# Optimization experiments

Measured on AMD Instinct MI355X. Metric: run time of the kernel, lower is better.

## Reference

```python
import jax, jax.numpy as jnp
import numpy as np

N_NODES = 10000
N_EDGES = 160000
MAX_K = 8
IN_NF = 64
HID = 64
ED = 16
HEADS = 4
NVEC = 5

def _mlp2_silu(x, w1, b1, w2, b2):
    # Linear -> SiLU -> Linear -> SiLU
    return jax.nn.silu(jax.nn.silu(x @ w1 + b1) @ w2 + b2)

def _mlp_out(x, w1, b1, w2, b2):
    # Linear -> SiLU -> Linear
    return jax.nn.silu(x @ w1 + b1) @ w2 + b2

def _segment_mean(data, ids, n):
    s = jax.ops.segment_sum(data, ids, num_segments=n)
    c = jax.ops.segment_sum(jnp.ones_like(data), ids, num_segments=n)
    return s / jnp.maximum(c, 1.0)

def setup_inputs() -> dict:
    key = jax.random.key(0)
    ks = jax.random.split(key, 48)
    p = lambda k, shape: jax.random.normal(k, shape, dtype=jnp.float32) * 0.05
    inp = {
        "h": jax.random.normal(ks[0], (N_NODES, IN_NF), dtype=jnp.float32),
        "coord": jax.random.normal(ks[1], (N_NODES, 3), dtype=jnp.float32),
        "edges": jax.random.randint(ks[2], (2, N_EDGES), 0, N_NODES),
        "nvecs": jax.random.normal(ks[3], (N_NODES, NVEC, 3), dtype=jnp.float32),
        "edge_attr": jax.random.normal(ks[4], (N_EDGES, ED), dtype=jnp.float32),
        "node_attr": jax.random.normal(ks[5], (N_NODES, HID), dtype=jnp.float32),
        "init_coord": jax.random.normal(ks[6], (N_NODES, 3), dtype=jnp.float32),
    }
    kidx = jax.random.randint(ks[7], (N_EDGES, 2, MAX_K), 0, N_EDGES)
    red = jax.random.uniform(ks[8], (N_EDGES, MAX_K)) < 0.2
    inp["klist"] = jnp.where(red[:, None, :], -1, kidx)
    chem_in = 2 * IN_NF + 2 * HID + ED
    pos_in = NVEC + 15 + ED  # edge_coords_nf(20) + edges_in_d
    inp.update({
        "w_chem1": p(ks[9], (chem_in, HID)), "b_chem1": jnp.zeros((HID,), jnp.float32),
        "w_chem2": p(ks[10], (HID, HID)), "b_chem2": jnp.zeros((HID,), jnp.float32),
        "w_pos1": p(ks[11], (pos_in, HID)), "b_pos1": jnp.zeros((HID,), jnp.float32),
        "w_pos2": p(ks[12], (HID, HID)), "b_pos2": jnp.zeros((HID,), jnp.float32),
        "w_sh": p(ks[13], (HID, HID)), "b_sh": jnp.zeros((HID,), jnp.float32),
        "w_att": p(ks[14], (HID, 1)), "b_att": jnp.zeros((1,), jnp.float32),
        "wq": p(ks[15], (HEADS, HID, HID)),
        "wk": p(ks[16], (HEADS, HID, HID)),
        "wv": p(ks[17], (HEADS, HID, HID)),
        "wb": p(ks[18], (HEADS, HID)),
        "wg": p(ks[19], (HEADS, HID, HID)), "bg": jnp.zeros((HEADS, HID), jnp.float32),
        "w_out": p(ks[20], (HEADS * HID, HID)), "b_out": jnp.zeros((HID,), jnp.float32),
        "wu1": p(ks[21], (HID, HID)), "bu1": jnp.zeros((HID,), jnp.float32),
        "wu2": p(ks[22], (HID, 1)), "bu2": jnp.zeros((1,), jnp.float32),
        "wx1": p(ks[23], (HID, HID)), "bx1": jnp.zeros((HID,), jnp.float32),
        "wx2": p(ks[24], (HID, 1)), "bx2": jnp.zeros((1,), jnp.float32),
        "wh1": p(ks[25], (2 * HID + IN_NF, HID)), "bh1": jnp.zeros((HID,), jnp.float32),
        "wh2": p(ks[26], (HID, HID)), "bh2": jnp.zeros((HID,), jnp.float32),
    })
    return inp

def reference(h, coord, edges, nvecs, edge_attr, node_attr, init_coord, klist,
              w_chem1, b_chem1, w_chem2, b_chem2, w_pos1, b_pos1, w_pos2, b_pos2,
              w_sh, b_sh, w_att, b_att, wq, wk, wv, wb, wg, bg, w_out, b_out,
              wu1, bu1, wu2, bu2, wx1, bx1, wx2, bx2, wh1, bh1, wh2, bh2):
    row, col = edges[0], edges[1]
    # radial features + normalized coordinate differences
    cd = coord[row] - coord[col]
    cd = cd / (jnp.linalg.norm(cd, axis=-1, keepdims=True) + 1e-8)
    init_radial = jnp.sum(cd ** 2, axis=1, keepdims=True)                 # (E, 1)
    radial = jnp.exp(init_radial * (-0.5 / 2.25 ** jnp.arange(15.0)))     # (E, 15)
    nprod = jnp.sum(nvecs[row] * nvecs[col], axis=-1)                     # (E, NVEC)
    chem = _mlp2_silu(jnp.concatenate([h[row], h[col], node_attr[row], node_attr[col], edge_attr], axis=1),
                      w_chem1, b_chem1, w_chem2, b_chem2)
    pos = _mlp2_silu(jnp.concatenate([nprod, radial, edge_attr], axis=1),
                     w_pos1, b_pos1, w_pos2, b_pos2)
    z = jax.nn.silu(chem @ w_sh + b_sh) * pos
    z = z * jax.nn.sigmoid(z @ w_att + b_att)
    # triangle k-NN attention over edges
    idx_i2k, idx_j2k = klist[:, 0], klist[:, 1]                           # (E, K)
    red = idx_i2k == -1
    heads = []
    for hd in range(HEADS):
        q = z @ wq[hd]; k_ = z @ wk[hd]; v = z @ wv[hd]; b = z @ wb[hd]
        g = jax.nn.sigmoid(z @ wg[hd] + bg[hd])
        tri_k = jnp.where(red[:, :, None], 0.0, k_[idx_i2k])              # (E, K, HID)
        tri_b = jnp.where(red, 0.0, b[idx_j2k])                           # (E, K)
        tri_v = v[idx_i2k]                                                # (E, K, HID)
        alpha = jnp.einsum('ed,ekd->ek', q, tri_k) / np.sqrt(HID) + tri_b
        alpha = jax.nn.softmax(jnp.where(red, -10000.0, alpha), axis=1)
        heads.append(g * jnp.einsum('ek,ekd->ed', alpha, tri_v))
    m = jnp.concatenate(heads, axis=-1) @ w_out + b_out
    # equivariant coordinate update
    ita = 0.2
    x_trans = cd * (_mlp_out(chem, wu1, bu1, wu2, bu2) * _mlp_out(pos, wx1, bx1, wx2, bx2))
    x_agg = _segment_mean(x_trans, row, N_NODES)
    coord_new = ita * init_coord + (1.0 - ita) * coord + x_agg
    m_agg = _segment_mean(m, row, N_NODES)
    h_new = h + _mlp_out(jnp.concatenate([h, node_attr, m_agg], axis=-1), wh1, bh1, wh2, bh2)
    return (h_new, coord_new)
```

## Files before the change

kernel.cpp:

```cpp
#include <hip/hip_runtime.h>
#include <math.h>

#define NE 160000
#define NN 10000

#define DEV __device__ __forceinline__

typedef float v2f __attribute__((ext_vector_type(2)));
typedef __attribute__((ext_vector_type(8))) short bf16x8;
typedef __attribute__((ext_vector_type(4))) float f32x4;

DEV float fsilu(float x) { return x / (1.0f + __expf(-x)); }
DEV float fsig(float x)  { return 1.0f / (1.0f + __expf(-x)); }

DEV unsigned pack2(float a, float b) {
  unsigned ua = __float_as_uint(a); ua += 0x7FFFu + ((ua >> 16) & 1u);
  unsigned ub = __float_as_uint(b); ub += 0x7FFFu + ((ub >> 16) & 1u);
  return (ua >> 16) | (ub & 0xFFFF0000u);
}

DEV unsigned packf8_4(float a, float b, float c, float d) {
  int r = __builtin_amdgcn_cvt_pk_fp8_f32(a, b, 0, false);
  r = __builtin_amdgcn_cvt_pk_fp8_f32(c, d, r, true);
  return (unsigned)r;
}
template<bool HI>
DEV v2f up2(unsigned u) { return __builtin_amdgcn_cvt_pk_f32_fp8((int)u, HI); }

DEV float dot16p(uint4 u, const float* q) {
  v2f f; float a = 0.f, b = 0.f;
  f = up2<false>(u.x); a = fmaf(f.x, q[0],  a); b = fmaf(f.y, q[1],  b);
  f = up2<true >(u.x); a = fmaf(f.x, q[2],  a); b = fmaf(f.y, q[3],  b);
  f = up2<false>(u.y); a = fmaf(f.x, q[4],  a); b = fmaf(f.y, q[5],  b);
  f = up2<true >(u.y); a = fmaf(f.x, q[6],  a); b = fmaf(f.y, q[7],  b);
  f = up2<false>(u.z); a = fmaf(f.x, q[8],  a); b = fmaf(f.y, q[9],  b);
  f = up2<true >(u.z); a = fmaf(f.x, q[10], a); b = fmaf(f.y, q[11], b);
  f = up2<false>(u.w); a = fmaf(f.x, q[12], a); b = fmaf(f.y, q[13], b);
  f = up2<true >(u.w); a = fmaf(f.x, q[14], a); b = fmaf(f.y, q[15], b);
  return a + b;
}
DEV void acc16(uint4 u, float pk, float* o) {
  v2f f;
  f = up2<false>(u.x); o[0]  = fmaf(pk, f.x, o[0]);  o[1]  = fmaf(pk, f.y, o[1]);
  f = up2<true >(u.x); o[2]  = fmaf(pk, f.x, o[2]);  o[3]  = fmaf(pk, f.y, o[3]);
  f = up2<false>(u.y); o[4]  = fmaf(pk, f.x, o[4]);  o[5]  = fmaf(pk, f.y, o[5]);
  f = up2<true >(u.y); o[6]  = fmaf(pk, f.x, o[6]);  o[7]  = fmaf(pk, f.y, o[7]);
  f = up2<false>(u.z); o[8]  = fmaf(pk, f.x, o[8]);  o[9]  = fmaf(pk, f.y, o[9]);
  f = up2<true >(u.z); o[10] = fmaf(pk, f.x, o[10]); o[11] = fmaf(pk, f.y, o[11]);
  f = up2<false>(u.w); o[12] = fmaf(pk, f.x, o[12]); o[13] = fmaf(pk, f.y, o[13]);
  f = up2<true >(u.w); o[14] = fmaf(pk, f.x, o[14]); o[15] = fmaf(pk, f.y, o[15]);
}

DEV void ldrow16(const unsigned* __restrict__ p, unsigned (&r)[16]) {
#pragma unroll
  for (int t = 0; t < 4; ++t) {
    uint4 u = ((const uint4*)p)[t];
    r[4*t] = u.x; r[4*t+1] = u.y; r[4*t+2] = u.z; r[4*t+3] = u.w;
  }
}
DEV void unpackf8_32(const unsigned (&p)[8], float (&o)[32]) {
#pragma unroll
  for (int t = 0; t < 8; ++t) {
    v2f f0 = up2<false>(p[t]);
    v2f f1 = up2<true >(p[t]);
    o[4*t+0] = f0.x; o[4*t+1] = f0.y; o[4*t+2] = f1.x; o[4*t+3] = f1.y;
  }
}
DEV void store32(float* dst, const float (&a)[32]) {
#pragma unroll
  for (int j = 0; j < 32; j += 4)
    *(float4*)(dst + j) = make_float4(a[j], a[j+1], a[j+2], a[j+3]);
}

DEV bf16x8 packrow8(const float* __restrict__ p) {
  float4 a = *(const float4*)p;
  float4 b = *(const float4*)(p + 4);
  uint4 u = make_uint4(pack2(a.x, a.y), pack2(a.z, a.w),
                       pack2(b.x, b.y), pack2(b.z, b.w));
  return __builtin_bit_cast(bf16x8, u);
}

DEV void mm4(const unsigned short* __restrict__ wm, int er, int q,
             const bf16x8 (&bfr)[2], f32x4 (&acc)[4]) {
#pragma unroll
  for (int nf = 0; nf < 4; ++nf) {
    const unsigned short* ar = wm + (size_t)(nf * 16 + er) * 64 + q * 8;
    const bf16x8 a0 = *(const bf16x8*)ar;
    const bf16x8 a1 = *(const bf16x8*)(ar + 32);
    acc[nf] = __builtin_amdgcn_mfma_f32_16x16x32_bf16(a0, bfr[0], acc[nf], 0, 0, 0);
    acc[nf] = __builtin_amdgcn_mfma_f32_16x16x32_bf16(a1, bfr[1], acc[nf], 0, 0, 0);
  }
}

__global__ void __launch_bounds__(256)
k_count(const int* __restrict__ edges, int* __restrict__ icnt) {
  int e = blockIdx.x * 256 + threadIdx.x;
  if (e < NE) atomicAdd(&icnt[edges[e]], 1);
}

__global__ void __launch_bounds__(256)
k_scan(const int* __restrict__ icnt, int* __restrict__ ioffs) {
  __shared__ int part[256];
  const int t = threadIdx.x;
  const int base = t * 40;
  int loc[40];
  int s = 0;
#pragma unroll
  for (int i = 0; i < 40; ++i) {
    int idx = base + i;
    int v = (idx < NN) ? icnt[idx] : 0;
    loc[i] = v; s += v;
  }
  part[t] = s;
  __syncthreads();
  for (int off = 1; off < 256; off <<= 1) {
    int v = (t >= off) ? part[t - off] : 0;
    __syncthreads();
    part[t] += v;
    __syncthreads();
  }
  int run = (t == 0) ? 0 : part[t - 1];
#pragma unroll
  for (int i = 0; i < 40; ++i) {
    int idx = base + i;
    if (idx < NN) { ioffs[idx] = run; run += loc[i]; }
  }
  if (t == 255) ioffs[NN] = NE;
}

__global__ void __launch_bounds__(256)
k_fill(const int* __restrict__ edges, const int* __restrict__ ioffs,
       int* __restrict__ icur, int* __restrict__ eidx) {
  int e = blockIdx.x * 256 + threadIdx.x;
  if (e >= NE) return;
  int r = edges[e];
  int p = atomicAdd(&icur[r], 1);
  eidx[ioffs[r] + p] = e;
}

__global__ void __launch_bounds__(256)
k_chem1m(const float* __restrict__ h, const float* __restrict__ na,
         const float* __restrict__ ea, const int* __restrict__ edges,
         const unsigned short* __restrict__ wtb, const float* __restrict__ b1,
         float* __restrict__ act1c) {
  const int lane = threadIdx.x & 63;
  const int wid  = threadIdx.x >> 6;
  const int er   = lane & 15;
  const int q    = lane >> 4;
  const int e    = blockIdx.x * 64 + wid * 16 + er;
  const int r = edges[e], c = edges[NE + e];

  const f32x4 zero = {0.f, 0.f, 0.f, 0.f};
  f32x4 acc[4] = {zero, zero, zero, zero};
  bf16x8 f[2];
  const float* xr;
  xr = h  + (size_t)r * 64; f[0] = packrow8(xr + q * 8); f[1] = packrow8(xr + 32 + q * 8);
  mm4(wtb + (size_t)29 * 4096, er, q, f, acc);
  xr = h  + (size_t)c * 64; f[0] = packrow8(xr + q * 8); f[1] = packrow8(xr + 32 + q * 8);
  mm4(wtb + (size_t)30 * 4096, er, q, f, acc);
  xr = na + (size_t)r * 64; f[0] = packrow8(xr + q * 8); f[1] = packrow8(xr + 32 + q * 8);
  mm4(wtb + (size_t)31 * 4096, er, q, f, acc);
  xr = na + (size_t)c * 64; f[0] = packrow8(xr + q * 8); f[1] = packrow8(xr + 32 + q * 8);
  mm4(wtb + (size_t)32 * 4096, er, q, f, acc);
  {
    bf16x8 ef;
    if (q < 2) ef = packrow8(ea + (size_t)e * 16 + q * 8);
    else { uint4 z4 = make_uint4(0, 0, 0, 0); ef = __builtin_bit_cast(bf16x8, z4); }
    const unsigned short* wm = wtb + (size_t)33 * 4096;
#pragma unroll
    for (int nf = 0; nf < 4; ++nf) {
      const bf16x8 a0 = *(const bf16x8*)(wm + (size_t)(nf * 16 + er) * 64 + q * 8);
      acc[nf] = __builtin_amdgcn_mfma_f32_16x16x32_bf16(a0, ef, acc[nf], 0, 0, 0);
    }
  }
#pragma unroll
  for (int nf = 0; nf < 4; ++nf) {
    const float4 b4 = *(const float4*)(b1 + nf * 16 + q * 4);
    *(float4*)(act1c + (size_t)e * 64 + nf * 16 + q * 4) =
        make_float4(fsilu(acc[nf].x + b4.x), fsilu(acc[nf].y + b4.y),
                    fsilu(acc[nf].z + b4.z), fsilu(acc[nf].w + b4.w));
  }
}

__global__ void __launch_bounds__(256)
k_pos1(const float* __restrict__ coord, const float* __restrict__ nv,
       const float* __restrict__ ea, const int* __restrict__ edges,
       const float* __restrict__ w1, const float* __restrict__ b1,
       float* __restrict__ act1p) {
  const int e = blockIdx.x * 256 + threadIdx.x;
  const int co = blockIdx.y * 32;
  const int r = edges[e], c = edges[NE + e];

  float dx = coord[r * 3 + 0] - coord[c * 3 + 0];
  float dy = coord[r * 3 + 1] - coord[c * 3 + 1];
  float dz = coord[r * 3 + 2] - coord[c * 3 + 2];
  float nrm = sqrtf(dx * dx + dy * dy + dz * dz);
  float inv = 1.0f / (nrm + 1e-8f);
  dx *= inv; dy *= inv; dz *= inv;
  float ir = dx * dx + dy * dy + dz * dz;

  float in[36];
#pragma unroll
  for (int v = 0; v < 5; ++v) {
    float s = 0.f;
#pragma unroll
    for (int d = 0; d < 3; ++d)
      s += nv[(size_t)r * 15 + v * 3 + d] * nv[(size_t)c * 15 + v * 3 + d];
    in[v] = s;
  }
  {
    float cexp = -0.5f;
#pragma unroll
    for (int k = 0; k < 15; ++k) { in[5 + k] = __expf(ir * cexp); cexp *= (1.0f / 2.25f); }
  }
#pragma unroll
  for (int k = 0; k < 16; k += 4) {
    float4 e4 = *(const float4*)(ea + (size_t)e * 16 + k);
    in[20 + k] = e4.x; in[21 + k] = e4.y; in[22 + k] = e4.z; in[23 + k] = e4.w;
  }

  float acc[32];
#pragma unroll
  for (int j = 0; j < 32; ++j) acc[j] = b1[co + j];
#pragma unroll
  for (int k = 0; k < 36; ++k) {
    const float x = in[k];
    const float* wr = w1 + (size_t)k * 64 + co;
#pragma unroll
    for (int j = 0; j < 32; ++j) acc[j] = fmaf(x, wr[j], acc[j]);
  }
#pragma unroll
  for (int j = 0; j < 32; ++j) acc[j] = fsilu(acc[j]);
  store32(act1p + (size_t)e * 64 + co, acc);
}

__global__ void __launch_bounds__(256)
k_wprep(const float* __restrict__ wk, const float* __restrict__ wv,
        const float* __restrict__ wq, const float* __restrict__ wg,
        const float* __restrict__ wsh, const float* __restrict__ wu1,
        const float* __restrict__ wx1, const float* __restrict__ wout,
        const float* __restrict__ wh1, const float* __restrict__ wh2,
        const float* __restrict__ w2c, const float* __restrict__ w2p,
        const float* __restrict__ wc1,
        unsigned short* __restrict__ wtb) {
  const int m = blockIdx.x;
  const float* src;
  bool pad16 = false, permk = false;
  if (m < 16) {
    const int hd = m >> 2, which = m & 3;
    src = ((which == 0) ? wk : (which == 1) ? wv : (which == 2) ? wq : wg)
          + (size_t)hd * 4096;
  } else if (m < 19) {
    src = (m == 16) ? wsh : (m == 17) ? wu1 : wx1;
  } else if (m < 23) {
    src = wout + (size_t)(m - 19) * 4096;
    permk = true;
  } else if (m < 26) {
    src = wh1 + (size_t)(m - 23) * 4096;
  } else if (m == 26) {
    src = wh2;
  } else if (m == 27) {
    src = w2c;
  } else if (m == 28) {
    src = w2p;
  } else if (m < 33) {
    src = wc1 + (size_t)(m - 29) * 4096;
  } else {
    src = wc1 + (size_t)4 * 4096;
    pad16 = true;
  }
  const int t = threadIdx.x;
#pragma unroll
  for (int i = 0; i < 16; ++i) {
    int idx = t * 16 + i;
    int n = idx >> 6, kk = idx & 63;
    int kr = permk ? (((kk >> 2) & 3) * 16 + (kk >> 4) * 4 + (kk & 3)) : kk;
    float v = (pad16 && kr >= 16) ? 0.f : src[kr * 64 + n];
    unsigned u = __float_as_uint(v);
    u += 0x7FFFu + ((u >> 16) & 1u);
    wtb[(size_t)m * 4096 + idx] = (unsigned short)(u >> 16);
  }
}

__global__ void __launch_bounds__(256)
k_l2s(const float* __restrict__ coord, const int* __restrict__ edges,
      const float* __restrict__ act1c, const float* __restrict__ act1p,
      const unsigned short* __restrict__ wtb,
      const float* __restrict__ b2c, const float* __restrict__ b2p,
      const float* __restrict__ bsh,
      const float* __restrict__ watt, const float* __restrict__ batt,
      const float* __restrict__ bu1, const float* __restrict__ wu2,
      const float* __restrict__ bu2,
      const float* __restrict__ bx1, const float* __restrict__ wx2,
      const float* __restrict__ bx2,
      const float* __restrict__ wb,
      unsigned* __restrict__ zb, float* __restrict__ be,
      float* __restrict__ x_sum, float* __restrict__ cntf) {
  __shared__ float ltc[4][16][68];
  __shared__ float ltp[4][16][68];
  const int lane = threadIdx.x & 63;
  const int wid  = threadIdx.x >> 6;
  const int er   = lane & 15;
  const int q    = lane >> 4;
  const int e    = blockIdx.x * 64 + wid * 16 + er;

  const f32x4 zero = {0.f, 0.f, 0.f, 0.f};
  bf16x8 f[2];

  {
    const float* xr = act1c + (size_t)e * 64;
    f[0] = packrow8(xr + q * 8); f[1] = packrow8(xr + 32 + q * 8);
  }
  f32x4 cD[4] = {zero, zero, zero, zero};
  mm4(wtb + (size_t)27 * 4096, er, q, f, cD);
#pragma unroll
  for (int nf = 0; nf < 4; ++nf) {
    const float4 bc = *(const float4*)(b2c + nf * 16 + q * 4);
    *(float4*)&ltc[wid][er][nf * 16 + q * 4] =
        make_float4(fsilu(cD[nf].x + bc.x), fsilu(cD[nf].y + bc.y),
                    fsilu(cD[nf].z + bc.z), fsilu(cD[nf].w + bc.w));
  }
  {
    const float* xr = act1p + (size_t)e * 64;
    f[0] = packrow8(xr + q * 8); f[1] = packrow8(xr + 32 + q * 8);
  }
  f32x4 pD[4] = {zero, zero, zero, zero};
  mm4(wtb + (size_t)28 * 4096, er, q, f, pD);
  float pv[16];
#pragma unroll
  for (int nf = 0; nf < 4; ++nf) {
    const float4 bp = *(const float4*)(b2p + nf * 16 + q * 4);
    pv[4*nf+0] = fsilu(pD[nf].x + bp.x); pv[4*nf+1] = fsilu(pD[nf].y + bp.y);
    pv[4*nf+2] = fsilu(pD[nf].z + bp.z); pv[4*nf+3] = fsilu(pD[nf].w + bp.w);
    *(float4*)&ltp[wid][er][nf * 16 + q * 4] =
        make_float4(pv[4*nf+0], pv[4*nf+1], pv[4*nf+2], pv[4*nf+3]);
  }
  bf16x8 cf[2], pf[2];
  cf[0] = packrow8(&ltc[wid][er][q * 8]); cf[1] = packrow8(&ltc[wid][er][32 + q * 8]);
  pf[0] = packrow8(&ltp[wid][er][q * 8]); pf[1] = packrow8(&ltp[wid][er][32 + q * 8]);

  float z[16];
  {
    f32x4 acc[4] = {zero, zero, zero, zero};
    mm4(wtb + (size_t)16 * 4096, er, q, cf, acc);
#pragma unroll
    for (int nf = 0; nf < 4; ++nf) {
      const float4 b4 = *(const float4*)(bsh + nf * 16 + q * 4);
      z[4*nf+0] = fsilu(acc[nf].x + b4.x) * pv[4*nf+0];
      z[4*nf+1] = fsilu(acc[nf].y + b4.y) * pv[4*nf+1];
      z[4*nf+2] = fsilu(acc[nf].z + b4.z) * pv[4*nf+2];
      z[4*nf+3] = fsilu(acc[nf].w + b4.w) * pv[4*nf+3];
    }
  }
  {
    float ap = 0.f;
#pragma unroll
    for (int nf = 0; nf < 4; ++nf)
#pragma unroll
      for (int r = 0; r < 4; ++r)
        ap = fmaf(z[4*nf+r], watt[nf * 16 + q * 4 + r], ap);
    ap += __shfl_xor(ap, 16);
    ap += __shfl_xor(ap, 32);
    const float sg = fsig(ap + batt[0]);
#pragma unroll
    for (int j = 0; j < 16; ++j) z[j] *= sg;
  }
  {
    unsigned* zrow = zb + (size_t)e * 32 + q * 2;
#pragma unroll
    for (int nf = 0; nf < 4; ++nf) {
      uint2 w = make_uint2(pack2(z[4*nf+0], z[4*nf+1]), pack2(z[4*nf+2], z[4*nf+3]));
      *(uint2*)(zrow + nf * 8) = w;
    }
  }
  {
    float bb[4];
#pragma unroll
    for (int hd = 0; hd < 4; ++hd) {
      float b = 0.f;
#pragma unroll
      for (int nf = 0; nf < 4; ++nf)
#pragma unroll
        for (int r = 0; r < 4; ++r)
          b = fmaf(z[4*nf+r], wb[hd * 64 + nf * 16 + q * 4 + r], b);
      b += __shfl_xor(b, 16);
      b += __shfl_xor(b, 32);
      bb[hd] = b;
    }
    if (q == 0)
      *(float4*)(be + (size_t)e * 4) = make_float4(bb[0], bb[1], bb[2], bb[3]);
  }
  float u;
  {
    f32x4 acc[4] = {zero, zero, zero, zero};
    mm4(wtb + (size_t)17 * 4096, er, q, cf, acc);
    float up = 0.f;
#pragma unroll
    for (int nf = 0; nf < 4; ++nf) {
      const float4 b4 = *(const float4*)(bu1 + nf * 16 + q * 4);
      const float4 w4 = *(const float4*)(wu2 + nf * 16 + q * 4);
      up = fmaf(fsilu(acc[nf].x + b4.x), w4.x, up);
      up = fmaf(fsilu(acc[nf].y + b4.y), w4.y, up);
      up = fmaf(fsilu(acc[nf].z + b4.z), w4.z, up);
      up = fmaf(fsilu(acc[nf].w + b4.w), w4.w, up);
    }
    up += __shfl_xor(up, 16);
    up += __shfl_xor(up, 32);
    u = up + bu2[0];
  }
  float xs;
  {
    f32x4 acc[4] = {zero, zero, zero, zero};
    mm4(wtb + (size_t)18 * 4096, er, q, pf, acc);
    float xp = 0.f;
#pragma unroll
    for (int nf = 0; nf < 4; ++nf) {
      const float4 b4 = *(const float4*)(bx1 + nf * 16 + q * 4);
      const float4 w4 = *(const float4*)(wx2 + nf * 16 + q * 4);
      xp = fmaf(fsilu(acc[nf].x + b4.x), w4.x, xp);
      xp = fmaf(fsilu(acc[nf].y + b4.y), w4.y, xp);
      xp = fmaf(fsilu(acc[nf].z + b4.z), w4.z, xp);
      xp = fmaf(fsilu(acc[nf].w + b4.w), w4.w, xp);
    }
    xp += __shfl_xor(xp, 16);
    xp += __shfl_xor(xp, 32);
    xs = xp + bx2[0];
  }

  if (q == 0) {
    const int r = edges[e], c = edges[NE + e];
    float dx = coord[r * 3 + 0] - coord[c * 3 + 0];
    float dy = coord[r * 3 + 1] - coord[c * 3 + 1];
    float dz = coord[r * 3 + 2] - coord[c * 3 + 2];
    float nrm = sqrtf(dx * dx + dy * dy + dz * dz);
    float inv = 1.0f / (nrm + 1e-8f);
    float t = u * xs;
    atomicAdd(&x_sum[r * 3 + 0], dx * inv * t);
    atomicAdd(&x_sum[r * 3 + 1], dy * inv * t);
    atomicAdd(&x_sum[r * 3 + 2], dz * inv * t);
    atomicAdd(&cntf[r], 1.0f);
  }
}

__global__ void __launch_bounds__(256)
k_projm(const unsigned* __restrict__ zb, const unsigned short* __restrict__ wtb,
        const float* __restrict__ bg,
        unsigned* __restrict__ ksep, unsigned* __restrict__ vsep,
        unsigned* __restrict__ qho, unsigned* __restrict__ gf8) {
  const int lane = threadIdx.x & 63;
  const int wid  = threadIdx.x >> 6;
  const int er   = lane & 15;
  const int q    = lane >> 4;
  const int e0   = blockIdx.x * 128 + wid * 32 + er;

  bf16x8 zf[2][2];
#pragma unroll
  for (int et = 0; et < 2; ++et) {
    const unsigned* zrow = zb + (size_t)(e0 + et * 16) * 32;
    zf[et][0] = __builtin_bit_cast(bf16x8, *(const uint4*)(zrow + q * 4));
    zf[et][1] = __builtin_bit_cast(bf16x8, *(const uint4*)(zrow + 16 + q * 4));
  }

  const f32x4 zero = {0.f, 0.f, 0.f, 0.f};
#pragma unroll 1
  for (int m = 0; m < 16; ++m) {
    const unsigned short* wm = wtb + (size_t)m * 4096;
    f32x4 acc[2][4];
#pragma unroll
    for (int et = 0; et < 2; ++et)
#pragma unroll
      for (int nf = 0; nf < 4; ++nf) acc[et][nf] = zero;
#pragma unroll
    for (int nf = 0; nf < 4; ++nf) {
      const unsigned short* ar = wm + (size_t)(nf * 16 + er) * 64 + q * 8;
      const bf16x8 a0 = *(const bf16x8*)ar;
      const bf16x8 a1 = *(const bf16x8*)(ar + 32);
#pragma unroll
      for (int et = 0; et < 2; ++et) {
        acc[et][nf] = __builtin_amdgcn_mfma_f32_16x16x32_bf16(a0, zf[et][0], acc[et][nf], 0, 0, 0);
        acc[et][nf] = __builtin_amdgcn_mfma_f32_16x16x32_bf16(a1, zf[et][1], acc[et][nf], 0, 0, 0);
      }
    }
    const int hd = m >> 2, which = m & 3;
#pragma unroll
    for (int et = 0; et < 2; ++et) {
      const size_t rec = (size_t)(e0 + et * 16) * 4 + hd;
      unsigned* dst = (which == 0) ? (ksep + rec * 16)
                    : (which == 1) ? (vsep + rec * 16)
                    : (which == 2) ? (qho + rec * 16)
                                   : (gf8 + rec * 16);
      unsigned pk[4];
      if (which == 3) {
#pragma unroll
        for (int nf = 0; nf < 4; ++nf) {
          const float4 b4 = *(const float4*)(bg + hd * 64 + nf * 16 + q * 4);
          pk[nf] = packf8_4(fsig(acc[et][nf].x + b4.x), fsig(acc[et][nf].y + b4.y),
                            fsig(acc[et][nf].z + b4.z), fsig(acc[et][nf].w + b4.w));
        }
      } else {
#pragma unroll
        for (int nf = 0; nf < 4; ++nf)
          pk[nf] = packf8_4(acc[et][nf].x, acc[et][nf].y,
                            acc[et][nf].z, acc[et][nf].w);
      }
      *(uint4*)(dst + q * 4) = make_uint4(pk[0], pk[1], pk[2], pk[3]);
    }
  }
}

__global__ void __launch_bounds__(256)
k_attnm(const unsigned* __restrict__ qho, const unsigned* __restrict__ gf8,
        const unsigned* __restrict__ ksep, const unsigned* __restrict__ vsep,
        const float* __restrict__ be, const int* __restrict__ klist,
        const unsigned short* __restrict__ wtb, float* __restrict__ medge) {
  __shared__ unsigned hl[128 * 33 + 4];
  const int tid = threadIdx.x;
  const int gt = blockIdx.x * 256 + tid;
  const int e = gt >> 3;
  const int hd = (gt >> 1) & 3, half = gt & 1;
  const int t = e * 4 + hd;

  float q[32];
  {
    unsigned qp[8];
    const uint4* qr = (const uint4*)(qho + (size_t)t * 16 + half * 8);
    uint4 a = qr[0], b = qr[1];
    qp[0] = a.x; qp[1] = a.y; qp[2] = a.z; qp[3] = a.w;
    qp[4] = b.x; qp[5] = b.y; qp[6] = b.z; qp[7] = b.w;
    unpackf8_32(qp, q);
  }

  int i2[8], j2[8];
#pragma unroll
  for (int kn = 0; kn < 8; ++kn) {
    i2[kn] = klist[(size_t)e * 16 + kn];
    j2[kn] = klist[(size_t)e * 16 + 8 + kn];
  }
  float bv[8];
#pragma unroll
  for (int kn = 0; kn < 8; ++kn)
    bv[kn] = be[(size_t)((i2[kn] < 0) ? 0 : j2[kn]) * 4 + hd];

  const uint4* k4 = (const uint4*)ksep;
  float alpha[8];
#pragma unroll 2
  for (int kn = 0; kn < 8; ++kn) {
    float d = 0.f;
    if (i2[kn] >= 0) {
      const uint4* kr = k4 + ((size_t)i2[kn] * 4 + hd) * 4 + half * 2;
      uint4 u0 = kr[0], u1 = kr[1];
      d = dot16p(u0, q) + dot16p(u1, q + 16);
    }
    d += __shfl_xor(d, 1);
    alpha[kn] = (i2[kn] < 0) ? -10000.0f : fmaf(d, 0.125f, bv[kn]);
  }
  float mx = alpha[0];
#pragma unroll
  for (int kn = 1; kn < 8; ++kn) mx = fmaxf(mx, alpha[kn]);
  float p[8], s = 0.f;
#pragma unroll
  for (int kn = 0; kn < 8; ++kn) { p[kn] = __expf(alpha[kn] - mx); s += p[kn]; }
  float is = 1.0f / s;
#pragma unroll
  for (int kn = 0; kn < 8; ++kn) p[kn] *= is;

  float ov[32];
#pragma unroll
  for (int j = 0; j < 32; ++j) ov[j] = 0.f;
  const uint4* v4 = (const uint4*)vsep;
#pragma unroll 2
  for (int kn = 0; kn < 8; ++kn) {
    int vi = (i2[kn] < 0) ? (NE - 1) : i2[kn];
    const uint4* vr = v4 + ((size_t)vi * 4 + hd) * 4 + half * 2;
    uint4 u0 = vr[0], u1 = vr[1];
    const float pk = p[kn];
    acc16(u0, pk, ov);
    acc16(u1, pk, ov + 16);
  }
  {
    unsigned gp[8];
    const uint4* gr = (const uint4*)(gf8 + (size_t)t * 16 + half * 8);
    uint4 a = gr[0], b = gr[1];
    gp[0] = a.x; gp[1] = a.y; gp[2] = a.z; gp[3] = a.w;
    gp[4] = b.x; gp[5] = b.y; gp[6] = b.z; gp[7] = b.w;
    float g[32];
    unpackf8_32(gp, g);
#pragma unroll
    for (int j = 0; j < 32; ++j) ov[j] *= g[j];
    const int r = (tid >> 3) * 4 + hd;
    unsigned* hw = hl + r * 33 + ((r >> 2) & 3) + half * 16;
#pragma unroll
    for (int j = 0; j < 16; ++j) hw[j] = pack2(ov[2*j], ov[2*j+1]);
  }
  __syncthreads();

  const int lane = tid & 63;
  const int w    = tid >> 6;
  if (w < 2) {
    const int er   = lane & 15;
    const int qq   = lane >> 4;
    const int eg   = blockIdx.x * 32 + w * 16 + er;

    const f32x4 zero = {0.f, 0.f, 0.f, 0.f};
    f32x4 acc[4] = {zero, zero, zero, zero};
#pragma unroll 1
    for (int hd2 = 0; hd2 < 4; ++hd2) {
      const int r = (w * 16 + er) * 4 + hd2;
      const unsigned* hr = hl + r * 33 + ((r >> 2) & 3);
      uint4 u0 = make_uint4(hr[qq*4], hr[qq*4+1], hr[qq*4+2], hr[qq*4+3]);
      uint4 u1 = make_uint4(hr[16+qq*4], hr[16+qq*4+1], hr[16+qq*4+2], hr[16+qq*4+3]);
      const bf16x8 hf0 = __builtin_bit_cast(bf16x8, u0);
      const bf16x8 hf1 = __builtin_bit_cast(bf16x8, u1);
      const unsigned short* wm = wtb + (size_t)(19 + hd2) * 4096;
#pragma unroll
      for (int nf = 0; nf < 4; ++nf) {
        const unsigned short* ar = wm + (size_t)(nf * 16 + er) * 64 + qq * 8;
        const bf16x8 a0 = *(const bf16x8*)ar;
        const bf16x8 a1 = *(const bf16x8*)(ar + 32);
        acc[nf] = __builtin_amdgcn_mfma_f32_16x16x32_bf16(a0, hf0, acc[nf], 0, 0, 0);
        acc[nf] = __builtin_amdgcn_mfma_f32_16x16x32_bf16(a1, hf1, acc[nf], 0, 0, 0);
      }
    }
#pragma unroll
    for (int nf = 0; nf < 4; ++nf)
      *(float4*)(medge + (size_t)eg * 64 + nf * 16 + qq * 4) =
          make_float4(acc[nf].x, acc[nf].y, acc[nf].z, acc[nf].w);
  }
}

__global__ void __launch_bounds__(256)
k_nodesum(const float* __restrict__ medge, const int* __restrict__ ioffs,
          const int* __restrict__ eidx, float* __restrict__ m_sum) {
  const int wid = threadIdx.x >> 6, lane = threadIdx.x & 63;
  const int n = blockIdx.x * 4 + wid;
  if (n >= NN) return;
  const int beg = ioffs[n], end = ioffs[n + 1];
  float acc = 0.f;
  for (int i = beg; i < end; ++i) {
    int e = eidx[i];
    acc += medge[(size_t)e * 64 + lane];
  }
  m_sum[(size_t)n * 64 + lane] = acc;
}

__global__ void __launch_bounds__(256)
k_finm(const float* __restrict__ h, const float* __restrict__ na,
       const float* __restrict__ coord, const float* __restrict__ icoord,
       const float* __restrict__ m_sum, const float* __restrict__ x_sum,
       const float* __restrict__ cntf, const float* __restrict__ bout,
       const unsigned short* __restrict__ wtb,
       const float* __restrict__ bh1, const float* __restrict__ bh2,
       float* __restrict__ out) {
  __shared__ float lt[4][16][68];
  const int lane = threadIdx.x & 63;
  const int wid  = threadIdx.x >> 6;
  const int er   = lane & 15;
  const int q    = lane >> 4;
  const int e    = blockIdx.x * 64 + wid * 16 + er;
  const bool valid = e < NN;
  const int el = valid ? e : 0;

  const float* hr = h + (size_t)el * 64;
  const float* nr = na + (size_t)el * 64;
  const float* mr = m_sum + (size_t)el * 64;
  const float cn = cntf[el];
  const float invc = 1.0f / fmaxf(cn, 1.0f);
  const float bsc = (cn > 0.f) ? 1.0f : 0.0f;

  bf16x8 hf[2], naf[2], mf[2];
  hf[0]  = packrow8(hr + q * 8); hf[1]  = packrow8(hr + 32 + q * 8);
  naf[0] = packrow8(nr + q * 8); naf[1] = packrow8(nr + 32 + q * 8);
#pragma unroll
  for (int half = 0; half < 2; ++half) {
    const int o = half * 32 + q * 8;
    const float4 m0 = *(const float4*)(mr + o);
    const float4 m1 = *(const float4*)(mr + o + 4);
    const float4 b0 = *(const float4*)(bout + o);
    const float4 b1 = *(const float4*)(bout + o + 4);
    float ma[8];
    ma[0] = fmaf(m0.x, invc, b0.x * bsc); ma[1] = fmaf(m0.y, invc, b0.y * bsc);
    ma[2] = fmaf(m0.z, invc, b0.z * bsc); ma[3] = fmaf(m0.w, invc, b0.w * bsc);
    ma[4] = fmaf(m1.x, invc, b1.x * bsc); ma[5] = fmaf(m1.y, invc, b1.y * bsc);
    ma[6] = fmaf(m1.z, invc, b1.z * bsc); ma[7] = fmaf(m1.w, invc, b1.w * bsc);
    uint4 u = make_uint4(pack2(ma[0], ma[1]), pack2(ma[2], ma[3]),
                         pack2(ma[4], ma[5]), pack2(ma[6], ma[7]));
    mf[half] = __builtin_bit_cast(bf16x8, u);
  }

  const f32x4 zero = {0.f, 0.f, 0.f, 0.f};
  f32x4 acc[4] = {zero, zero, zero, zero};
  mm4(wtb + (size_t)23 * 4096, er, q, hf,  acc);
  mm4(wtb + (size_t)24 * 4096, er, q, naf, acc);
  mm4(wtb + (size_t)25 * 4096, er, q, mf,  acc);
#pragma unroll
  for (int nf = 0; nf < 4; ++nf) {
    const float4 b4 = *(const float4*)(bh1 + nf * 16 + q * 4);
    float* d = &lt[wid][er][nf * 16 + q * 4];
    d[0] = fsilu(acc[nf].x + b4.x); d[1] = fsilu(acc[nf].y + b4.y);
    d[2] = fsilu(acc[nf].z + b4.z); d[3] = fsilu(acc[nf].w + b4.w);
  }
  __syncthreads();
  bf16x8 sf[2];
  sf[0] = packrow8(&lt[wid][er][q * 8]);
  sf[1] = packrow8(&lt[wid][er][32 + q * 8]);
  f32x4 a2[4] = {zero, zero, zero, zero};
  mm4(wtb + (size_t)26 * 4096, er, q, sf, a2);
  if (valid) {
#pragma unroll
    for (int nf = 0; nf < 4; ++nf) {
      const float4 b4 = *(const float4*)(bh2 + nf * 16 + q * 4);
      const float4 h4 = *(const float4*)(hr + nf * 16 + q * 4);
      *(float4*)(out + (size_t)e * 64 + nf * 16 + q * 4) =
          make_float4(a2[nf].x + b4.x + h4.x, a2[nf].y + b4.y + h4.y,
                      a2[nf].z + b4.z + h4.z, a2[nf].w + b4.w + h4.w);
    }
    if (q == 0) {
#pragma unroll
      for (int d = 0; d < 3; ++d)
        out[(size_t)NN * 64 + e * 3 + d] =
            0.2f * icoord[e * 3 + d] + 0.8f * coord[e * 3 + d] + x_sum[e * 3 + d] * invc;
    }
  }
}

extern "C" void kernel_launch(void* const* d_in, const int* in_sizes, int n_in,
                              void* d_out, int out_size, void* d_ws, size_t ws_size,
                              hipStream_t stream) {
  (void)in_sizes; (void)n_in; (void)out_size; (void)ws_size;
  const float* h      = (const float*)d_in[0];
  const float* coord  = (const float*)d_in[1];
  const int*   edges  = (const int*)  d_in[2];
  const float* nvecs  = (const float*)d_in[3];
  const float* ea     = (const float*)d_in[4];
  const float* na     = (const float*)d_in[5];
  const float* icoord = (const float*)d_in[6];
  const int*   klist  = (const int*)  d_in[7];
  const float* w_chem1 = (const float*)d_in[8];
  const float* b_chem1 = (const float*)d_in[9];
  const float* w_chem2 = (const float*)d_in[10];
  const float* b_chem2 = (const float*)d_in[11];
  const float* w_pos1  = (const float*)d_in[12];
  const float* b_pos1  = (const float*)d_in[13];
  const float* w_pos2  = (const float*)d_in[14];
  const float* b_pos2  = (const float*)d_in[15];
  const float* w_sh    = (const float*)d_in[16];
  const float* b_sh    = (const float*)d_in[17];
  const float* w_att   = (const float*)d_in[18];
  const float* b_att   = (const float*)d_in[19];
  const float* wq      = (const float*)d_in[20];
  const float* wk      = (const float*)d_in[21];
  const float* wv      = (const float*)d_in[22];
  const float* wb      = (const float*)d_in[23];
  const float* wg      = (const float*)d_in[24];
  const float* bg      = (const float*)d_in[25];
  const float* w_out   = (const float*)d_in[26];
  const float* b_out   = (const float*)d_in[27];
  const float* wu1     = (const float*)d_in[28];
  const float* bu1     = (const float*)d_in[29];
  const float* wu2     = (const float*)d_in[30];
  const float* bu2     = (const float*)d_in[31];
  const float* wx1     = (const float*)d_in[32];
  const float* bx1     = (const float*)d_in[33];
  const float* wx2     = (const float*)d_in[34];
  const float* bx2     = (const float*)d_in[35];
  const float* wh1     = (const float*)d_in[36];
  const float* bh1     = (const float*)d_in[37];
  const float* wh2     = (const float*)d_in[38];
  const float* bh2     = (const float*)d_in[39];

  float* out = (float*)d_out;
  float* ws  = (float*)d_ws;
  float* R1 = ws;
  float* R2 = R1 + (size_t)NE * 64;
  float* R3 = R2 + (size_t)NE * 64;
  float* R4 = R3 + (size_t)NE * 64;
  float* zbf   = R4 + (size_t)NE * 64;
  float* x_sum = zbf + (size_t)NE * 32;
  float* cntf  = x_sum + (size_t)NN * 3;
  int*   icnt  = (int*)(cntf + NN);
  int*   icur  = icnt + NN;
  float* m_sum = (float*)(icur + NN);
  float* be    = m_sum + (size_t)NN * 64;
  unsigned short* wtb = (unsigned short*)(be + (size_t)4 * NE);
  int*   ioffs = (int*)(wtb + 34 * 4096);
  int*   eidx  = ioffs + (NN + 1);

  unsigned* ksep = (unsigned*)R1;
  unsigned* vsep = (unsigned*)R2;
  unsigned* qho  = (unsigned*)R3;
  unsigned* gf8  = (unsigned*)R4;
  unsigned* zb   = (unsigned*)zbf;
  float* medge = R3;

  (void)hipMemsetAsync(x_sum, 0, ((size_t)NN * 3 + NN + NN + NN) * sizeof(float), stream);

  dim3 b256(256);
  dim3 gflat(NE / 256);

  k_wprep<<<dim3(34), b256, 0, stream>>>(wk, wv, wq, wg, w_sh, wu1, wx1, w_out,
                                         wh1, wh2, w_chem2, w_pos2, w_chem1, wtb);
  k_count<<<gflat, b256, 0, stream>>>(edges, icnt);
  k_scan <<<dim3(1), b256, 0, stream>>>(icnt, ioffs);
  k_fill <<<gflat, b256, 0, stream>>>(edges, ioffs, icur, eidx);

  k_chem1m<<<dim3(NE / 64), b256, 0, stream>>>(h, na, ea, edges, wtb, b_chem1, R1);
  k_pos1  <<<dim3(NE / 256, 2), b256, 0, stream>>>(coord, nvecs, ea, edges, w_pos1, b_pos1, R2);
  k_l2s   <<<dim3(NE / 64), b256, 0, stream>>>(coord, edges, R1, R2, wtb,
                                               b_chem2, b_pos2, b_sh, w_att, b_att,
                                               bu1, wu2, bu2, bx1, wx2, bx2, wb,
                                               zb, be, x_sum, cntf);
  k_projm<<<dim3(NE / 128), b256, 0, stream>>>(zb, wtb, bg, ksep, vsep, qho, gf8);
  k_attnm<<<dim3(NE * 8 / 256), b256, 0, stream>>>(qho, gf8, ksep, vsep, be, klist,
                                                   wtb, medge);
  k_nodesum<<<dim3((NN + 3) / 4), b256, 0, stream>>>(medge, ioffs, eidx, m_sum);
  k_finm<<<dim3((NN + 63) / 64), b256, 0, stream>>>(h, na, coord, icoord, m_sum, x_sum,
                                                    cntf, b_out, wtb, bh1, bh2, out);
}
```

Baseline: 601.0 us.

## Split attention head work across four lanes instead of two per edge-head

The triangle-attention kernel now assigns each (edge, head) pair to four threads, each handling 16 of the 64 channels. The half-dot products are combined with an extra shuffle, and twice as many blocks are launched, each covering 16 edges. The goal is more parallelism and fewer registers per thread, which should raise occupancy and help hide the latency of the gathered K/V loads. The cost is duplicated klist and bias loads across more lanes, an extra shuffle, and only one wave per block doing the output MFMA.

Result: no change. 602.2 us (+0.2%).

```diff
diff --git a/kernel.cpp b/kernel.cpp
--- a/kernel.cpp
+++ b/kernel.cpp
@@ -51,16 +51,10 @@
   f = up2<true >(u.w); o[14] = fmaf(pk, f.x, o[14]); o[15] = fmaf(pk, f.y, o[15]);
 }
 
-DEV void ldrow16(const unsigned* __restrict__ p, unsigned (&r)[16]) {
+DEV void unpackf8_16(uint4 a, float (&o)[16]) {
+  unsigned p[4] = {a.x, a.y, a.z, a.w};
 #pragma unroll
   for (int t = 0; t < 4; ++t) {
-    uint4 u = ((const uint4*)p)[t];
-    r[4*t] = u.x; r[4*t+1] = u.y; r[4*t+2] = u.z; r[4*t+3] = u.w;
-  }
-}
-DEV void unpackf8_32(const unsigned (&p)[8], float (&o)[32]) {
-#pragma unroll
-  for (int t = 0; t < 8; ++t) {
     v2f f0 = up2<false>(p[t]);
     v2f f1 = up2<true >(p[t]);
     o[4*t+0] = f0.x; o[4*t+1] = f0.y; o[4*t+2] = f1.x; o[4*t+3] = f1.y;
@@ -513,33 +507,24 @@
         const unsigned* __restrict__ ksep, const unsigned* __restrict__ vsep,
         const float* __restrict__ be, const int* __restrict__ klist,
         const unsigned short* __restrict__ wtb, float* __restrict__ medge) {
-  __shared__ unsigned hl[128 * 33 + 4];
+  __shared__ unsigned hl[64 * 33 + 4];
   const int tid = threadIdx.x;
   const int gt = blockIdx.x * 256 + tid;
-  const int e = gt >> 3;
-  const int hd = (gt >> 1) & 3, half = gt & 1;
+  const int e = gt >> 4;
+  const int hd = (gt >> 2) & 3, quar = gt & 3;
   const int t = e * 4 + hd;
 
-  float q[32];
-  {
-    unsigned qp[8];
-    const uint4* qr = (const uint4*)(qho + (size_t)t * 16 + half * 8);
-    uint4 a = qr[0], b = qr[1];
-    qp[0] = a.x; qp[1] = a.y; qp[2] = a.z; qp[3] = a.w;
-    qp[4] = b.x; qp[5] = b.y; qp[6] = b.z; qp[7] = b.w;
-    unpackf8_32(qp, q);
-  }
-
-  int i2[8], j2[8];
+  float q[16];
+  unpackf8_16(*(const uint4*)(qho + (size_t)t * 16 + quar * 4), q);
+
+  int i2[8];
+  float bv[8];
 #pragma unroll
   for (int kn = 0; kn < 8; ++kn) {
     i2[kn] = klist[(size_t)e * 16 + kn];
-    j2[kn] = klist[(size_t)e * 16 + 8 + kn];
-  }
-  float bv[8];
-#pragma unroll
-  for (int kn = 0; kn < 8; ++kn)
-    bv[kn] = be[(size_t)((i2[kn] < 0) ? 0 : j2[kn]) * 4 + hd];
+    int j2 = klist[(size_t)e * 16 + 8 + kn];
+    bv[kn] = be[(size_t)((i2[kn] < 0) ? 0 : j2) * 4 + hd];
+  }
 
   const uint4* k4 = (const uint4*)ksep;
   float alpha[8];
@@ -547,11 +532,11 @@
   for (int kn = 0; kn < 8; ++kn) {
     float d = 0.f;
     if (i2[kn] >= 0) {
-      const uint4* kr = k4 + ((size_t)i2[kn] * 4 + hd) * 4 + half * 2;
-      uint4 u0 = kr[0], u1 = kr[1];
-      d = dot16p(u0, q) + dot16p(u1, q + 16);
+      const uint4 u0 = k4[((size_t)i2[kn] * 4 + hd) * 4 + quar];
+      d = dot16p(u0, q);
     }
     d += __shfl_xor(d, 1);
+    d += __shfl_xor(d, 2);
     alpha[kn] = (i2[kn] < 0) ? -10000.0f : fmaf(d, 0.125f, bv[kn]);
   }
   float mx = alpha[0];
@@ -564,48 +549,38 @@
 #pragma unroll
   for (int kn = 0; kn < 8; ++kn) p[kn] *= is;
 
-  float ov[32];
-#pragma unroll
-  for (int j = 0; j < 32; ++j) ov[j] = 0.f;
+  float ov[16];
+#pragma unroll
+  for (int j = 0; j < 16; ++j) ov[j] = 0.f;
   const uint4* v4 = (const uint4*)vsep;
 #pragma unroll 2
   for (int kn = 0; kn < 8; ++kn) {
     int vi = (i2[kn] < 0) ? (NE - 1) : i2[kn];
-    const uint4* vr = v4 + ((size_t)vi * 4 + hd) * 4 + half * 2;
-    uint4 u0 = vr[0], u1 = vr[1];
-    const float pk = p[kn];
-    acc16(u0, pk, ov);
-    acc16(u1, pk, ov + 16);
-  }
-  {
-    unsigned gp[8];
-    const uint4* gr = (const uint4*)(gf8 + (size_t)t * 16 + half * 8);
-    uint4 a = gr[0], b = gr[1];
-    gp[0] = a.x; gp[1] = a.y; gp[2] = a.z; gp[3] = a.w;
-    gp[4] = b.x; gp[5] = b.y; gp[6] = b.z; gp[7] = b.w;
-    float g[32];
-    unpackf8_32(gp, g);
-#pragma unroll
-    for (int j = 0; j < 32; ++j) ov[j] *= g[j];
-    const int r = (tid >> 3) * 4 + hd;
-    unsigned* hw = hl + r * 33 + ((r >> 2) & 3) + half * 16;
-#pragma unroll
-    for (int j = 0; j < 16; ++j) hw[j] = pack2(ov[2*j], ov[2*j+1]);
+    const uint4 u0 = v4[((size_t)vi * 4 + hd) * 4 + quar];
+    acc16(u0, p[kn], ov);
+  }
+  {
+    float g[16];
+    unpackf8_16(*(const uint4*)(gf8 + (size_t)t * 16 + quar * 4), g);
+#pragma unroll
+    for (int j = 0; j < 16; ++j) ov[j] *= g[j];
+    const int r = (tid >> 4) * 4 + hd;
+    unsigned* hw = hl + r * 33 + ((r >> 2) & 3) + quar * 8;
+#pragma unroll
+    for (int j = 0; j < 8; ++j) hw[j] = pack2(ov[2*j], ov[2*j+1]);
   }
   __syncthreads();
 
-  const int lane = tid & 63;
-  const int w    = tid >> 6;
-  if (w < 2) {
-    const int er   = lane & 15;
-    const int qq   = lane >> 4;
-    const int eg   = blockIdx.x * 32 + w * 16 + er;
+  if (tid < 64) {
+    const int er   = tid & 15;
+    const int qq   = tid >> 4;
+    const int eg   = blockIdx.x * 16 + er;
 
     const f32x4 zero = {0.f, 0.f, 0.f, 0.f};
     f32x4 acc[4] = {zero, zero, zero, zero};
 #pragma unroll 1
     for (int hd2 = 0; hd2 < 4; ++hd2) {
-      const int r = (w * 16 + er) * 4 + hd2;
+      const int r = er * 4 + hd2;
       const unsigned* hr = hl + r * 33 + ((r >> 2) & 3);
       uint4 u0 = make_uint4(hr[qq*4], hr[qq*4+1], hr[qq*4+2], hr[qq*4+3]);
       uint4 u1 = make_uint4(hr[16+qq*4], hr[16+qq*4+1], hr[16+qq*4+2], hr[16+qq*4+3]);
@@ -810,8 +785,8 @@
                                                bu1, wu2, bu2, bx1, wx2, bx2, wb,
                                                zb, be, x_sum, cntf);
   k_projm<<<dim3(NE / 128), b256, 0, stream>>>(zb, wtb, bg, ksep, vsep, qho, gf8);
-  k_attnm<<<dim3(NE * 8 / 256), b256, 0, stream>>>(qho, gf8, ksep, vsep, be, klist,
-                                                   wtb, medge);
+  k_attnm<<<dim3(NE * 16 / 256), b256, 0, stream>>>(qho, gf8, ksep, vsep, be, klist,
+                                                    wtb, medge);
   k_nodesum<<<dim3((NN + 3) / 4), b256, 0, stream>>>(medge, ioffs, eidx, m_sum);
   k_finm<<<dim3((NN + 63) / 64), b256, 0, stream>>>(h, na, coord, icoord, m_sum, x_sum,
                                                     cntf, b_out, wtb, bh1, bh2, out);
```
